# Optimization experiments

Measured on AMD Instinct MI355X. Metric: run time of the kernel, lower is better.

Reference implementation:

```python
import jax, jax.numpy as jnp
import numpy as np

B, N, IN_DIM, OUT_DIM, H = 8, 1024, 512, 512, 8
SUP = OUT_DIM // H  # support_dim per head = 64


def setup_inputs() -> dict:
    key = jax.random.key(0)
    ks = jax.random.split(key, 6)
    # 0/1 dense adjacency with self-loops so no row is fully masked
    A = jax.random.randint(ks[0], (B, N, N), 0, 2).astype(jnp.float32)
    A = jnp.maximum(A, jnp.eye(N, dtype=jnp.float32)[None])
    X = jax.random.normal(ks[1], (B, N, IN_DIM), dtype=jnp.float32)
    # parameters, uniform(-1/sqrt(fan_last), 1/sqrt(fan_last)) as in reset_parameters
    sw = 1.0 / np.sqrt(SUP)
    W = jax.random.uniform(ks[2], (H, IN_DIM, SUP), minval=-sw, maxval=sw, dtype=jnp.float32)
    w1 = jax.random.uniform(ks[3], (H, SUP), minval=-sw, maxval=sw, dtype=jnp.float32)
    w2 = jax.random.uniform(ks[4], (H, SUP), minval=-sw, maxval=sw, dtype=jnp.float32)
    b = jax.random.uniform(ks[5], (2, H), minval=-1.0, maxval=1.0, dtype=jnp.float32)
    b1, b2 = b[0], b[1]
    return {"A": A, "X": X, "W": W, "w1": w1, "b1": b1, "w2": w2, "b2": b2}


def reference(A, X, W, w1, b1, w2, b2):
    # per-head projection: [B,H,N,SUP]
    inputs = jnp.einsum('bni,hio->bhno', X, W)
    # additive attention logits: self_fc [B,H,N,1] + neigh_fc [B,H,1,N]
    self_fc = jnp.einsum('bhno,ho->bhn', inputs, w1) + b1[None, :, None]
    neigh_fc = jnp.einsum('bhno,ho->bhn', inputs, w2) + b2[None, :, None]
    logits = jax.nn.leaky_relu(self_fc[..., :, None] + neigh_fc[..., None, :], 0.01)
    mask = -1e9 * (1.0 - A)  # [B,N,N]
    alphas = jax.nn.softmax(logits + mask[:, None], axis=-1)  # [B,H,N,N]
    out = jnp.einsum('bhnm,bhmo->bhno', alphas, inputs)
    out = jax.nn.relu(out)  # default activation = torch.relu
    # concat heads on last dim (head i contiguous), matching torch.cat
    return out.transpose(0, 2, 1, 3).reshape(B, N, H * SUP)
```

## Files before the change

### kernel.cpp

```cpp
#include <hip/hip_runtime.h>
#include <hip/hip_fp16.h>

#define BB 8
#define NN 1024
#define IN_DIM 512
#define HH 8
#define SUP 64
#define HS (HH * SUP)

#define XS_STRIDE 40
#define VT_STRIDE 136

typedef _Float16 half8 __attribute__((ext_vector_type(8)));
typedef _Float16 half2v __attribute__((ext_vector_type(2)));
typedef float floatx4 __attribute__((ext_vector_type(4)));

__global__ __launch_bounds__(256) void kW(const float* __restrict__ W,
                                          _Float16* __restrict__ Wt) {
    __shared__ float tile[64][65];
    const int it = blockIdx.x & 7;
    const int h  = blockIdx.x >> 3;
    const int t  = threadIdx.x;
    {
        const int i  = t >> 2;
        const int o0 = (t & 3) * 16;
        const float* src = W + ((size_t)h * IN_DIM + it * 64 + i) * SUP + o0;
#pragma unroll
        for (int j = 0; j < 4; j++) {
            float4 v = ((const float4*)src)[j];
            tile[i][o0 + j * 4 + 0] = v.x;
            tile[i][o0 + j * 4 + 1] = v.y;
            tile[i][o0 + j * 4 + 2] = v.z;
            tile[i][o0 + j * 4 + 3] = v.w;
        }
    }
    __syncthreads();
    {
        const int o  = t >> 2;
        const int i0 = (t & 3) * 16;
        _Float16 buf[16];
#pragma unroll
        for (int j = 0; j < 16; j++) buf[j] = (_Float16)tile[i0 + j][o];
        _Float16* dst = Wt + ((size_t)h * SUP + o) * IN_DIM + it * 64 + i0;
        *(half8*)dst       = *(half8*)buf;
        *(half8*)(dst + 8) = *(half8*)(buf + 8);
    }
}

__global__ __launch_bounds__(256) void k1_proj(const float* __restrict__ X,
                                               const _Float16* __restrict__ Wt,
                                               const float* __restrict__ A,
                                               unsigned char* __restrict__ Am,
                                               const float* __restrict__ w1,
                                               const float* __restrict__ b1,
                                               const float* __restrict__ w2,
                                               const float* __restrict__ b2,
                                               _Float16* __restrict__ Pt,
                                               float* __restrict__ s_g,
                                               float* __restrict__ t_g,
                                               float* __restrict__ tmax16) {
    __shared__ __align__(16) _Float16 xs[2][64 * XS_STRIDE];
    __shared__ __align__(16) _Float16 wsh[2][128 * XS_STRIDE];
    __shared__ __align__(16) _Float16 po[128 * 72];
    __shared__ float tred[2][64];

    const int bid  = blockIdx.x;
    const int t    = threadIdx.x;
    const int wave = t >> 6;
    const int lane = t & 63;

    if (bid >= 512) {
        const int idx = bid - 512;
#pragma unroll
        for (int i = 0; i < 8; i++) {
            const int row = idx * 32 + wave * 8 + i;
            const float* arow = A + (size_t)row * NN;
            unsigned long long keep = 0;
#pragma unroll
            for (int g = 0; g < 16; g++) {
                float a = arow[g * 64 + lane];
                unsigned long long bal = __ballot(a > 0.5f);
                if (lane == g) keep = bal;
            }
            if (lane < 16)
                *(unsigned long long*)(Am + (size_t)row * 128 + lane * 8) = keep;
        }
        return;
    }

    const int b    = bid & 7;
    const int j    = bid >> 3;
    const int h0   = (j & 3) * 2;
    const int bh0  = b * 8 + h0;
    const int n0   = (j >> 2) * 64;
    const int quad = lane >> 4;
    const int l15  = lane & 15;
    const int row  = t >> 2;
    const int koff = (t & 3) * 8;
    const int wrow  = t >> 1;
    const int wkoff = (t & 1) * 16;

    floatx4 acc[8];
#pragma unroll
    for (int i = 0; i < 8; i++) acc[i] = {0.f, 0.f, 0.f, 0.f};

    float w1v[8], w2v[8];
#pragma unroll
    for (int ct = 0; ct < 8; ct++) {
        w1v[ct] = w1[h0 * 64 + ct * 16 + l15];
        w2v[ct] = w2[h0 * 64 + ct * 16 + l15];
    }
    const float b1h0 = b1[h0], b1h1 = b1[h0 + 1];
    const float b2h0 = b2[h0], b2h1 = b2[h0 + 1];

    const float*    xbase = X + ((size_t)b * NN + n0 + row) * IN_DIM + koff;
    const _Float16* wbase = Wt + ((size_t)(h0 * SUP) + wrow) * IN_DIM + wkoff;

    float4 xa = ((const float4*)xbase)[0];
    float4 xb = ((const float4*)xbase)[1];
    half8  wv0 = ((const half8*)wbase)[0];
    half8  wv1 = *(const half8*)(wbase + 8);

    for (int it = 0; it < 16; it++) {
        const int cur = it & 1;
        {
            _Float16 xh[8] = {(_Float16)xa.x, (_Float16)xa.y, (_Float16)xa.z, (_Float16)xa.w,
                              (_Float16)xb.x, (_Float16)xb.y, (_Float16)xb.z, (_Float16)xb.w};
            *(half8*)&xs[cur][row * XS_STRIDE + koff] = *(half8*)xh;
            *(half8*)&wsh[cur][wrow * XS_STRIDE + wkoff]     = wv0;
            *(half8*)&wsh[cur][wrow * XS_STRIDE + wkoff + 8] = wv1;
        }
        __syncthreads();
        if (it < 15) {
            const float* src = xbase + (it + 1) * 32;
            xa = ((const float4*)src)[0];
            xb = ((const float4*)src)[1];
            wv0 = *(const half8*)(wbase + (it + 1) * 32);
            wv1 = *(const half8*)(wbase + (it + 1) * 32 + 8);
        }
        half8 af = *(const half8*)&xs[cur][(wave * 16 + l15) * XS_STRIDE + quad * 8];
#pragma unroll
        for (int ct = 0; ct < 8; ct++) {
            half8 bf = *(const half8*)&wsh[cur][(ct * 16 + l15) * XS_STRIDE + quad * 8];
            acc[ct] = __builtin_amdgcn_mfma_f32_16x16x32_f16(af, bf, acc[ct], 0, 0, 0);
        }
    }
    __syncthreads();

#pragma unroll
    for (int ct = 0; ct < 8; ct++) {
#pragma unroll
        for (int r = 0; r < 4; r++) {
            int o = ct * 16 + l15;
            int n = wave * 16 + quad * 4 + r;
            po[o * 72 + n] = (_Float16)acc[ct][r];
        }
    }
#pragma unroll
    for (int r = 0; r < 4; r++) {
        float sp0 = 0.f, tp0 = 0.f, sp1 = 0.f, tp1 = 0.f;
#pragma unroll
        for (int ct = 0; ct < 4; ct++) {
            sp0 += acc[ct][r] * w1v[ct];
            tp0 += acc[ct][r] * w2v[ct];
            sp1 += acc[ct + 4][r] * w1v[ct + 4];
            tp1 += acc[ct + 4][r] * w2v[ct + 4];
        }
#pragma unroll
        for (int off = 1; off < 16; off <<= 1) {
            sp0 += __shfl_xor(sp0, off);
            tp0 += __shfl_xor(tp0, off);
            sp1 += __shfl_xor(sp1, off);
            tp1 += __shfl_xor(tp1, off);
        }
        if (l15 == 0) {
            const int n = wave * 16 + quad * 4 + r;
            s_g[(size_t)bh0 * NN + n0 + n] = sp0 + b1h0;
            float tv0 = tp0 + b2h0;
            t_g[(size_t)bh0 * NN + n0 + n] = tv0;
            tred[0][n] = tv0;
            s_g[(size_t)(bh0 + 1) * NN + n0 + n] = sp1 + b1h1;
            float tv1 = tp1 + b2h1;
            t_g[(size_t)(bh0 + 1) * NN + n0 + n] = tv1;
            tred[1][n] = tv1;
        }
    }
    __syncthreads();
    {
        const int orow = t >> 1;
        const int nof  = (t & 1) * 32;
        _Float16* dst = Pt + ((size_t)(bh0 * SUP + orow)) * NN + n0 + nof;
        const _Float16* src = &po[orow * 72 + nof];
        *(half8*)dst        = *(const half8*)src;
        *(half8*)(dst + 8)  = *(const half8*)(src + 8);
        *(half8*)(dst + 16) = *(const half8*)(src + 16);
        *(half8*)(dst + 24) = *(const half8*)(src + 24);
    }
    if (t == 0) {
        float m0 = -1e30f, m1 = -1e30f;
#pragma unroll
        for (int i = 0; i < 64; i++) {
            m0 = fmaxf(m0, tred[0][i]);
            m1 = fmaxf(m1, tred[1][i]);
        }
        tmax16[bh0 * 16 + (n0 >> 6)] = m0;
        tmax16[(bh0 + 1) * 16 + (n0 >> 6)] = m1;
    }
}

__global__ __launch_bounds__(512) void k2_attn(const unsigned char* __restrict__ Am,
                                               const _Float16* __restrict__ Pt,
                                               const float* __restrict__ s_g,
                                               const float* __restrict__ t_g,
                                               const float* __restrict__ tmax16,
                                               float* __restrict__ out) {
    __shared__ __align__(16) _Float16 vts[2][64 * VT_STRIDE];
    __shared__ __align__(16) unsigned t2l[NN / 2];
    __shared__ __align__(16) uint4 lutm[256];

    const int bid = blockIdx.x;
    const int h   = bid & 7;
    const int b   = (bid >> 3) & 7;
    const int bh  = b * 8 + h;
    const int n0  = (bid >> 6) * 128;
    const int t    = threadIdx.x;
    const int wave = t >> 6;
    const int lane = t & 63;
    const int quad = lane >> 4;
    const int l15  = lane & 15;
    const int row4 = t >> 3;
    const int seg  = t & 7;

    {
        float2 tv2 = ((const float2*)(t_g + (size_t)bh * NN))[t];
        half2v tp = {(_Float16)tv2.x, (_Float16)tv2.y};
        t2l[t] = *(unsigned*)&tp;
    }
    if (t < 256) {
        unsigned e = (unsigned)t;
        uint4 v;
        v.x = ((e & 1u)   ? 0xFFFFu : 0u) | ((e & 2u)   ? 0xFFFF0000u : 0u);
        v.y = ((e & 4u)   ? 0xFFFFu : 0u) | ((e & 8u)   ? 0xFFFF0000u : 0u);
        v.z = ((e & 16u)  ? 0xFFFFu : 0u) | ((e & 32u)  ? 0xFFFF0000u : 0u);
        v.w = ((e & 64u)  ? 0xFFFFu : 0u) | ((e & 128u) ? 0xFFFF0000u : 0u);
        lutm[t] = v;
    }

    float tmax = -1e30f;
#pragma unroll
    for (int i = 0; i < 16; i++) tmax = fmaxf(tmax, tmax16[bh * 16 + i]);

    const int myrow = wave * 16 + l15;
    const float sv = s_g[(size_t)bh * NN + n0 + myrow];
    const float xc = sv + tmax;
    const float cv = fmaxf(xc, 0.01f * xc);
    const float l2e = 1.44269504f;
    const _Float16 sc1h = (_Float16)((sv - cv) * l2e);
    const _Float16 sc2h = (_Float16)(-0.99f * cv * l2e);
    const half2v sc1 = {sc1h, sc1h};
    const half2v sc2 = {sc2h, sc2h};
    const half2v vl2e = {(_Float16)l2e, (_Float16)l2e};
    const half2v v001 = {(_Float16)0.01f, (_Float16)0.01f};
    const half2v ones2 = {(_Float16)1.0f, (_Float16)1.0f};

    floatx4 acc[4];
#pragma unroll
    for (int i = 0; i < 4; i++) acc[i] = {0.f, 0.f, 0.f, 0.f};
    float zp = 0.f;

    const _Float16* pb = Pt + ((size_t)bh * SUP + row4) * NN + seg * 16;
    half8 v0 = ((const half8*)pb)[0];
    half8 v1 = ((const half8*)pb)[1];
    const uint4* mrow = (const uint4*)(Am + ((size_t)b * NN + n0 + myrow) * 128);
    uint4 mcur = mrow[0];

    for (int mt = 0; mt < 8; mt++) {
        const int cur = mt & 1;
        {
            _Float16* d = &vts[cur][row4 * VT_STRIDE + seg * 16];
            ((half8*)d)[0] = v0;
            ((half8*)d)[1] = v1;
        }
        __syncthreads();
        uint4 mnext;
        if (mt < 7) {
            const _Float16* p = pb + (mt + 1) * 128;
            v0 = ((const half8*)p)[0];
            v1 = ((const half8*)p)[1];
            mnext = mrow[mt + 1];
        }
        const unsigned mw[4] = {mcur.x, mcur.y, mcur.z, mcur.w};
#pragma unroll
        for (int kk = 0; kk < 4; kk++) {
            const unsigned mbyte = (mw[kk] >> (quad * 8)) & 0xffu;
            uint4 mx = lutm[mbyte];
            const unsigned mxw[4] = {mx.x, mx.y, mx.z, mx.w};
            uint4 tw = *(const uint4*)&t2l[mt * 64 + kk * 16 + quad * 4];
            union { uint4 u; half2v h[4]; } tt; tt.u = tw;
            union { half2v h[4]; half8 h8; } wbu;
#pragma unroll
            for (int p = 0; p < 4; p++) {
                half2v y = tt.h[p] * vl2e + sc1;
                half2v w = y * v001 + sc2;
                half2v z = __builtin_elementwise_max(y, w);
                __half2 zz = *(__half2*)&z;
                __half2 ee = h2exp2(zz);
                unsigned eb = (*(unsigned*)&ee) & mxw[p];
                half2v e2 = *(half2v*)&eb;
#if __has_builtin(__builtin_amdgcn_fdot2)
                zp = __builtin_amdgcn_fdot2(e2, ones2, zp, false);
#else
                zp += (float)e2.x + (float)e2.y;
#endif
                wbu.h[p] = e2;
            }
            half8 af = wbu.h8;
#pragma unroll
            for (int ct = 0; ct < 4; ct++) {
                half8 bf = *(const half8*)&vts[cur][(ct * 16 + l15) * VT_STRIDE + kk * 32 + quad * 8];
                acc[ct] = __builtin_amdgcn_mfma_f32_16x16x32_f16(af, bf, acc[ct], 0, 0, 0);
            }
        }
        if (mt < 7) mcur = mnext;
    }

    zp += __shfl_xor(zp, 16);
    zp += __shfl_xor(zp, 32);
    const float rzown = 1.0f / zp;

#pragma unroll
    for (int r = 0; r < 4; r++) {
        const int rr = wave * 16 + quad * 4 + r;
        const float rz = __shfl(rzown, quad * 20 + r);
#pragma unroll
        for (int ct = 0; ct < 4; ct++) {
            float v = acc[ct][r] * rz;
            v = v > 0.f ? v : 0.f;
            out[((size_t)b * NN + n0 + rr) * HS + h * SUP + ct * 16 + l15] = v;
        }
    }
}

extern "C" void kernel_launch(void* const* d_in, const int* in_sizes, int n_in,
                              void* d_out, int out_size, void* d_ws, size_t ws_size,
                              hipStream_t stream) {
    const float* A  = (const float*)d_in[0];
    const float* X  = (const float*)d_in[1];
    const float* W  = (const float*)d_in[2];
    const float* w1 = (const float*)d_in[3];
    const float* b1 = (const float*)d_in[4];
    const float* w2 = (const float*)d_in[5];
    const float* b2 = (const float*)d_in[6];
    float* out = (float*)d_out;

    char* ws = (char*)d_ws;
    _Float16*      Wt     = (_Float16*)(ws);
    _Float16*      Pt     = (_Float16*)(ws + 524288);
    float*         s_g    = (float*)(ws + 8912896);
    float*         t_g    = (float*)(ws + 9175040);
    float*         tmax16 = (float*)(ws + 9437184);
    unsigned char* Am     = (unsigned char*)(ws + 9441280);

    hipLaunchKernelGGL(kW, dim3(64), dim3(256), 0, stream, W, Wt);
    hipLaunchKernelGGL(k1_proj, dim3(768), dim3(256), 0, stream,
                       X, Wt, A, Am, w1, b1, w2, b2, Pt, s_g, t_g, tmax16);
    hipLaunchKernelGGL(k2_attn, dim3(512), dim3(512), 0, stream,
                       Am, Pt, s_g, t_g, tmax16, out);
}
```

Before: 132.9 us.

## Stage full per-head value matrix in LDS once with 1024-thread blocks

```diff
diff --git a/kernel.cpp b/kernel.cpp
--- a/kernel.cpp
+++ b/kernel.cpp
@@ -9,7 +9,7 @@
 #define HS (HH * SUP)
 
 #define XS_STRIDE 40
-#define VT_STRIDE 136
+#define VT2 1032
 
 typedef _Float16 half8 __attribute__((ext_vector_type(8)));
 typedef _Float16 half2v __attribute__((ext_vector_type(2)));
@@ -208,30 +208,48 @@
     }
 }
 
-__global__ __launch_bounds__(512) void k2_attn(const unsigned char* __restrict__ Am,
-                                               const _Float16* __restrict__ Pt,
-                                               const float* __restrict__ s_g,
-                                               const float* __restrict__ t_g,
-                                               const float* __restrict__ tmax16,
-                                               float* __restrict__ out) {
-    __shared__ __align__(16) _Float16 vts[2][64 * VT_STRIDE];
+__global__ __launch_bounds__(1024) void k2_attn(const unsigned char* __restrict__ Am,
+                                                const _Float16* __restrict__ Pt,
+                                                const float* __restrict__ s_g,
+                                                const float* __restrict__ t_g,
+                                                const float* __restrict__ tmax16,
+                                                float* __restrict__ out) {
+    __shared__ __align__(16) _Float16 vts[64 * VT2];
     __shared__ __align__(16) unsigned t2l[NN / 2];
     __shared__ __align__(16) uint4 lutm[256];
 
-    const int bid = blockIdx.x;
-    const int h   = bid & 7;
-    const int b   = (bid >> 3) & 7;
-    const int bh  = b * 8 + h;
-    const int n0  = (bid >> 6) * 128;
+    const int bid  = blockIdx.x;
+    const int b    = bid & 7;
+    const int rest = bid >> 3;
+    const int h    = rest & 7;
+    const int bh   = b * 8 + h;
+    const int n0   = (rest >> 3) * 256;
     const int t    = threadIdx.x;
     const int wave = t >> 6;
     const int lane = t & 63;
     const int quad = lane >> 4;
     const int l15  = lane & 15;
-    const int row4 = t >> 3;
-    const int seg  = t & 7;
 
     {
+        const int tt   = t & 511;
+        const int half = t >> 9;
+        const int row4 = tt >> 3;
+        const int seg  = tt & 7;
+        const _Float16* src = Pt + ((size_t)bh * SUP + row4) * NN + half * 512 + seg * 16;
+        _Float16*       dst = &vts[row4 * VT2 + half * 512 + seg * 16];
+        half8 r0[4], r1[4];
+#pragma unroll
+        for (int m = 0; m < 4; m++) {
+            r0[m] = ((const half8*)(src + m * 128))[0];
+            r1[m] = ((const half8*)(src + m * 128))[1];
+        }
+#pragma unroll
+        for (int m = 0; m < 4; m++) {
+            ((half8*)(dst + m * 128))[0] = r0[m];
+            ((half8*)(dst + m * 128))[1] = r1[m];
+        }
+    }
+    if (t < 512) {
         float2 tv2 = ((const float2*)(t_g + (size_t)bh * NN))[t];
         half2v tp = {(_Float16)tv2.x, (_Float16)tv2.y};
         t2l[t] = *(unsigned*)&tp;
@@ -268,27 +286,14 @@
     for (int i = 0; i < 4; i++) acc[i] = {0.f, 0.f, 0.f, 0.f};
     float zp = 0.f;
 
-    const _Float16* pb = Pt + ((size_t)bh * SUP + row4) * NN + seg * 16;
-    half8 v0 = ((const half8*)pb)[0];
-    half8 v1 = ((const half8*)pb)[1];
     const uint4* mrow = (const uint4*)(Am + ((size_t)b * NN + n0 + myrow) * 128);
     uint4 mcur = mrow[0];
 
+    __syncthreads();
+
     for (int mt = 0; mt < 8; mt++) {
-        const int cur = mt & 1;
-        {
-            _Float16* d = &vts[cur][row4 * VT_STRIDE + seg * 16];
-            ((half8*)d)[0] = v0;
-            ((half8*)d)[1] = v1;
-        }
-        __syncthreads();
         uint4 mnext;
-        if (mt < 7) {
-            const _Float16* p = pb + (mt + 1) * 128;
-            v0 = ((const half8*)p)[0];
-            v1 = ((const half8*)p)[1];
-            mnext = mrow[mt + 1];
-        }
+        if (mt < 7) mnext = mrow[mt + 1];
         const unsigned mw[4] = {mcur.x, mcur.y, mcur.z, mcur.w};
 #pragma unroll
         for (int kk = 0; kk < 4; kk++) {
@@ -317,7 +322,7 @@
             half8 af = wbu.h8;
 #pragma unroll
             for (int ct = 0; ct < 4; ct++) {
-                half8 bf = *(const half8*)&vts[cur][(ct * 16 + l15) * VT_STRIDE + kk * 32 + quad * 8];
+                half8 bf = *(const half8*)&vts[(ct * 16 + l15) * VT2 + mt * 128 + kk * 32 + quad * 8];
                 acc[ct] = __builtin_amdgcn_mfma_f32_16x16x32_f16(af, bf, acc[ct], 0, 0, 0);
             }
         }
@@ -364,6 +369,6 @@
     hipLaunchKernelGGL(kW, dim3(64), dim3(256), 0, stream, W, Wt);
     hipLaunchKernelGGL(k1_proj, dim3(768), dim3(256), 0, stream,
                        X, Wt, A, Am, w1, b1, w2, b2, Pt, s_g, t_g, tmax16);
-    hipLaunchKernelGGL(k2_attn, dim3(512), dim3(512), 0, stream,
+    hipLaunchKernelGGL(k2_attn, dim3(256), dim3(1024), 0, stream,
                        Am, Pt, s_g, t_g, tmax16, out);
 }
```

New measurement: 130.5 us. No clear change (-1.8%).
